# Kernel optimization log

Measured on AMD Instinct MI355X. Metric: run time of the kernel, lower is better.

Reference implementation:

```python
import jax, jax.numpy as jnp
import numpy as np

B, C, T, V, P = 32, 64, 512, 54, 4
EPS = 1e-5


def setup_inputs() -> dict:
    key = jax.random.key(0)
    ks = jax.random.split(key, 5)
    x = jax.random.normal(ks[0], (B, C, T, V), dtype=jnp.float32)
    A = jax.random.uniform(ks[1], (P, V, V), dtype=jnp.float32)
    gweights = jax.random.normal(ks[2], (P, V, V), dtype=jnp.float32)
    W = jax.random.normal(ks[3], (P, C, C), dtype=jnp.float32) * 0.05  # (P, C_out, C_in)
    b = jax.random.normal(ks[4], (P, C), dtype=jnp.float32) * 0.05
    gamma = jnp.ones((C,), dtype=jnp.float32)
    beta = jnp.zeros((C,), dtype=jnp.float32)
    return {"x": x, "A": A, "gweights": gweights, "W": W, "b": b,
            "gamma": gamma, "beta": beta}


def reference(x, A, gweights, W, b, gamma, beta):
    # x: (B, C_in, T, V)
    Aeff = A * gweights  # (P, V, V), learned-weighted adjacency
    # per-part graph aggregation (x @ A_p) followed by 1x1 conv, summed over parts
    # out[b,o,t,v] = sum_p sum_c sum_u x[b,c,t,u] * Aeff[p,u,v] * W[p,o,c] + sum_p b[p,o]
    y = jnp.einsum('bctu,puv,poc->botv', x, Aeff, W, optimize=True)
    y = y + jnp.sum(b, axis=0)[None, :, None, None]
    # BatchNorm2d in training mode: batch stats over (B, T, V) per channel
    mean = jnp.mean(y, axis=(0, 2, 3), keepdims=True)
    var = jnp.mean(jnp.square(y - mean), axis=(0, 2, 3), keepdims=True)
    y = (y - mean) * jax.lax.rsqrt(var + EPS)
    y = y * gamma[None, :, None, None] + beta[None, :, None, None]
    y = jax.nn.relu(y)
    # temporal_conv is Identity (kernel_size=None); residual shortcut is Identity (C_in==C_out)
    return y + x
```

## Files before the change

### kernel.cpp

```cpp
#include <hip/hip_runtime.h>
#include <hip/hip_bf16.h>


typedef __bf16 bf16_t;
typedef __bf16 bf16x8 __attribute__((ext_vector_type(8)));
typedef float  f32x4  __attribute__((ext_vector_type(4)));

#define XT_STRIDE 72
#define UP_STRIDE 232

static __device__ __forceinline__ f32x4 mfma16(bf16x8 a, bf16x8 b, f32x4 c) {
  return __builtin_amdgcn_mfma_f32_16x16x32_bf16(a, b, c, 0, 0, 0);
}

__global__ __launch_bounds__(256) void k_prep(
    const float* __restrict__ A, const float* __restrict__ g,
    const float* __restrict__ W, const float* __restrict__ bias,
    bf16_t* __restrict__ Wstk, bf16_t* __restrict__ At,
    float* __restrict__ bsum, float* __restrict__ stats) {
  int i = blockIdx.x * 256 + threadIdx.x;
  if (i < 16384) Wstk[i] = (bf16_t)W[i];
  if (i < 64 * 224) {
    int v = i / 224, pu = i - v * 224;
    float val = 0.f;
    if (v < 54 && pu < 216) { int idx = pu * 54 + v; val = A[idx] * g[idx]; }
    At[i] = (bf16_t)val;
  }
  if (i < 64) {
    float s = 0.f;
    for (int p = 0; p < 4; ++p) s += bias[p * 64 + i];
    bsum[i] = s;
  }
  if (i < 8192) stats[i] = 0.f;
}

__global__ __launch_bounds__(256) void k_pass1(
    const float* __restrict__ x, const bf16_t* __restrict__ Wstk,
    const bf16_t* __restrict__ At, const float* __restrict__ bsum,
    float* __restrict__ ypre, float* __restrict__ stats) {
  __shared__ bf16_t XtS[4 * 54 * XT_STRIDE];
  __shared__ bf16_t UpS[64 * UP_STRIDE];

  const int tid  = threadIdx.x;
  const int bid  = blockIdx.x;
  const int b    = bid >> 7;
  const int t0   = (bid & 127) << 2;
  const int w    = tid >> 6;
  const int L    = tid & 63;
  const int quad = L >> 4;
  const int l15  = L & 15;

  for (int i = tid; i < 64 * 8; i += 256)
    UpS[(i >> 3) * UP_STRIDE + 216 + (i & 7)] = (bf16_t)0.0f;

  const float* xb = x + (size_t)(b * 64 * 512 + t0) * 54;
  for (int j = tid; j < 64 * 216; j += 256) {
    int c = j / 216;
    int r = j - c * 216;
    float v = xb[(size_t)c * 27648 + r];
    int tt = r / 54;
    int u  = r - tt * 54;
    XtS[(tt * 54 + u) * XT_STRIDE + c] = (bf16_t)v;
  }

  bf16x8 wfr[4][2];
  #pragma unroll
  for (int mi = 0; mi < 4; ++mi) {
    const bf16_t* arow = Wstk + (((((w << 2) + mi) << 4) + l15) * 64) + (quad << 3);
    #pragma unroll
    for (int kk = 0; kk < 2; ++kk)
      wfr[mi][kk] = *(const bf16x8*)(arow + kk * 32);
  }

  const int obase = (w << 4) + (quad << 2);
  float bs[4];
  #pragma unroll
  for (int r = 0; r < 4; ++r) bs[r] = bsum[obase + r];

  bf16x8 zf;
  #pragma unroll
  for (int j = 0; j < 8; ++j) zf[j] = (bf16_t)0.0f;

  float ssum[4] = {0.f, 0.f, 0.f, 0.f};
  float ssq[4]  = {0.f, 0.f, 0.f, 0.f};

  __syncthreads();

  for (int tt = 0; tt < 4; ++tt) {
    bf16x8 xfr[4][2];
    #pragma unroll
    for (int nt = 0; nt < 4; ++nt) {
      const int urow = (nt << 4) + l15;
      #pragma unroll
      for (int kk = 0; kk < 2; ++kk) {
        xfr[nt][kk] = zf;
        if (urow < 54)
          xfr[nt][kk] = *(const bf16x8*)(&XtS[(tt * 54 + urow) * XT_STRIDE + kk * 32 + (quad << 3)]);
      }
    }
    #pragma unroll
    for (int mi = 0; mi < 4; ++mi) {
      f32x4 acc[4];
      #pragma unroll
      for (int nt = 0; nt < 4; ++nt)
        #pragma unroll
        for (int e = 0; e < 4; ++e) acc[nt][e] = 0.f;
      #pragma unroll
      for (int kk = 0; kk < 2; ++kk)
        #pragma unroll
        for (int nt = 0; nt < 4; ++nt)
          acc[nt] = mfma16(wfr[mi][kk], xfr[nt][kk], acc[nt]);
      #pragma unroll
      for (int nt = 0; nt < 4; ++nt) {
        const int u = (nt << 4) + l15;
        if (u < 54) {
          #pragma unroll
          for (int r = 0; r < 4; ++r) {
            int o = (mi << 4) + (quad << 2) + r;
            UpS[o * UP_STRIDE + w * 54 + u] = (bf16_t)acc[nt][r];
          }
        }
      }
    }
    __syncthreads();

    bf16x8 afr[7];
    #pragma unroll
    for (int kk = 0; kk < 7; ++kk)
      afr[kk] = *(const bf16x8*)(&UpS[((w << 4) + l15) * UP_STRIDE + kk * 32 + (quad << 3)]);
    f32x4 acc[4];
    #pragma unroll
    for (int nt = 0; nt < 4; ++nt)
      #pragma unroll
      for (int e = 0; e < 4; ++e) acc[nt][e] = 0.f;
    #pragma unroll
    for (int kk = 0; kk < 7; ++kk) {
      #pragma unroll
      for (int nt = 0; nt < 4; ++nt) {
        bf16x8 bfr = *(const bf16x8*)(At + ((nt << 4) + l15) * 224 + kk * 32 + (quad << 3));
        acc[nt] = mfma16(afr[kk], bfr, acc[nt]);
      }
    }
    const int t = t0 + tt;
    #pragma unroll
    for (int nt = 0; nt < 4; ++nt) {
      const int vcol = (nt << 4) + l15;
      if (vcol < 54) {
        #pragma unroll
        for (int r = 0; r < 4; ++r) {
          float yv = acc[nt][r] + bs[r];
          ypre[(((size_t)b * 64 + (obase + r)) * 512 + t) * 54 + vcol] = yv;
          ssum[r] += yv;
          ssq[r]  += yv * yv;
        }
      }
    }
    __syncthreads();
  }

  #pragma unroll
  for (int off = 1; off < 16; off <<= 1) {
    #pragma unroll
    for (int r = 0; r < 4; ++r) {
      ssum[r] += __shfl_xor(ssum[r], off);
      ssq[r]  += __shfl_xor(ssq[r], off);
    }
  }
  if (l15 == 0) {
    float* sb = stats + (bid & 63) * 128;
    #pragma unroll
    for (int r = 0; r < 4; ++r) {
      atomicAdd(&sb[obase + r], ssum[r]);
      atomicAdd(&sb[64 + obase + r], ssq[r]);
    }
  }
}

__global__ void k_finalize(const float* __restrict__ gamma, const float* __restrict__ beta,
                           const float* __restrict__ stats, float* __restrict__ ac) {
  int o = threadIdx.x;
  if (o >= 64) return;
  float S = 0.f, Q = 0.f;
  for (int buf = 0; buf < 64; ++buf) {
    S += stats[buf * 128 + o];
    Q += stats[buf * 128 + 64 + o];
  }
  const float inv = 1.0f / 884736.0f;
  float mean = S * inv;
  float var  = Q * inv - mean * mean;
  float a = gamma[o] * rsqrtf(var + 1e-5f);
  ac[o]      = a;
  ac[64 + o] = beta[o] - mean * a;
}

__global__ __launch_bounds__(256) void k_pass2(const float* __restrict__ x,
                                               const float* __restrict__ ac,
                                               float* __restrict__ out) {
  size_t i4 = (size_t)blockIdx.x * 256 + threadIdx.x;
  int o = (int)((i4 / 6912) & 63);
  float a = ac[o], c = ac[64 + o];
  float4 yp = ((const float4*)out)[i4];
  float4 xv = ((const float4*)x)[i4];
  float4 res;
  res.x = fmaxf(a * yp.x + c, 0.f) + xv.x;
  res.y = fmaxf(a * yp.y + c, 0.f) + xv.y;
  res.z = fmaxf(a * yp.z + c, 0.f) + xv.z;
  res.w = fmaxf(a * yp.w + c, 0.f) + xv.w;
  ((float4*)out)[i4] = res;
}

extern "C" void kernel_launch(void* const* d_in, const int* in_sizes, int n_in,
                              void* d_out, int out_size, void* d_ws, size_t ws_size,
                              hipStream_t stream) {
  const float* x     = (const float*)d_in[0];
  const float* A     = (const float*)d_in[1];
  const float* g     = (const float*)d_in[2];
  const float* W     = (const float*)d_in[3];
  const float* bias  = (const float*)d_in[4];
  const float* gamma = (const float*)d_in[5];
  const float* beta  = (const float*)d_in[6];

  char* ws = (char*)d_ws;
  bf16_t* Wstk = (bf16_t*)(ws + 0);
  bf16_t* At   = (bf16_t*)(ws + 32768);
  float*  bsum = (float*)(ws + 61440);
  float*  stats= (float*)(ws + 61696);
  float*  ac   = (float*)(ws + 94464);
  float*  out  = (float*)d_out;

  k_prep<<<64, 256, 0, stream>>>(A, g, W, bias, Wstk, At, bsum, stats);
  k_pass1<<<4096, 256, 0, stream>>>(x, Wstk, At, bsum, out, stats);
  k_finalize<<<1, 64, 0, stream>>>(gamma, beta, stats, ac);
  k_pass2<<<55296, 256, 0, stream>>>(x, ac, out);
}
```

Before: 619.6 us.

## Pre-transpose x to bf16 channel-last, store pre-BN output in bf16, restructure pass1

A new transpose kernel converts x into a bf16 (B, T*V, C) layout so pass1 can load MFMA fragments directly from global memory, with no strided fp32 gather or LDS transpose. Pass1 swaps MFMA operand roles, double-buffers the intermediate LDS tile, and writes the pre-normalisation activations as bf16 into workspace, which halves that intermediate traffic in pass1 and pass2. Which path runs depends on workspace size, with fp32 and legacy fallbacks kept. The cost is an extra pass over x plus bf16 rounding of the stored pre-BN values, which lowers accuracy.

```diff
diff --git a/kernel.cpp b/kernel.cpp
--- a/kernel.cpp
+++ b/kernel.cpp
@@ -4,13 +4,17 @@
 
 typedef __bf16 bf16_t;
 typedef __bf16 bf16x8 __attribute__((ext_vector_type(8)));
+typedef __bf16 bf16x4 __attribute__((ext_vector_type(4)));
 typedef float  f32x4  __attribute__((ext_vector_type(4)));
-
-#define XT_STRIDE 72
-#define UP_STRIDE 232
+typedef unsigned int uint32;
 
 static __device__ __forceinline__ f32x4 mfma16(bf16x8 a, bf16x8 b, f32x4 c) {
   return __builtin_amdgcn_mfma_f32_16x16x32_bf16(a, b, c, 0, 0, 0);
+}
+static __device__ __forceinline__ uint32 pk2(float a, float b) {
+  union { __bf16 h; unsigned short u; } ua, ub;
+  ua.h = (__bf16)a; ub.h = (__bf16)b;
+  return (uint32)ua.u | ((uint32)ub.u << 16);
 }
 
 __global__ __launch_bounds__(256) void k_prep(
@@ -34,12 +38,49 @@
   if (i < 8192) stats[i] = 0.f;
 }
 
+__global__ __launch_bounds__(256) void k_tr(const float* __restrict__ x,
+                                            bf16_t* __restrict__ xT) {
+  __shared__ bf16_t T[256 * 66];
+  const int tid = threadIdx.x;
+  const int b = blockIdx.x / 108;
+  const int rblk = blockIdx.x - b * 108;
+  const int r0 = rblk << 8;
+  const float* xb = x + (size_t)b * 64 * 27648 + r0;
+  #pragma unroll 4
+  for (int j = 0; j < 16; ++j) {
+    int idx = tid + (j << 8);
+    int c = idx >> 6, r4 = idx & 63;
+    const float* src = xb + (size_t)c * 27648 + r4;
+    #pragma unroll
+    for (int k = 0; k < 4; ++k) {
+      float v = src[k << 6];
+      T[(r4 + (k << 6)) * 66 + c] = (bf16_t)v;
+    }
+  }
+  __syncthreads();
+  bf16_t* outb = xT + (((size_t)b * 27648 + r0) << 6);
+  const uint32* Td = (const uint32*)T;
+  #pragma unroll
+  for (int j = 0; j < 8; ++j) {
+    int row = (tid >> 3) + (j << 5);
+    int seg = tid & 7;
+    uint32 d0 = Td[row * 33 + (seg << 2) + 0];
+    uint32 d1 = Td[row * 33 + (seg << 2) + 1];
+    uint32 d2 = Td[row * 33 + (seg << 2) + 2];
+    uint32 d3 = Td[row * 33 + (seg << 2) + 3];
+    uint4 vv = make_uint4(d0, d1, d2, d3);
+    *(uint4*)(outb + ((size_t)row << 6) + (seg << 3)) = vv;
+  }
+}
+
+#define UPS 232
+
+template<bool YBF16>
 __global__ __launch_bounds__(256) void k_pass1(
-    const float* __restrict__ x, const bf16_t* __restrict__ Wstk,
+    const bf16_t* __restrict__ xT, const bf16_t* __restrict__ Wstk,
     const bf16_t* __restrict__ At, const float* __restrict__ bsum,
-    float* __restrict__ ypre, float* __restrict__ stats) {
-  __shared__ bf16_t XtS[4 * 54 * XT_STRIDE];
-  __shared__ bf16_t UpS[64 * UP_STRIDE];
+    void* __restrict__ yprev, float* __restrict__ stats) {
+  __shared__ bf16_t UpS[2][64 * UPS];
 
   const int tid  = threadIdx.x;
   const int bid  = blockIdx.x;
@@ -50,42 +91,138 @@
   const int quad = L >> 4;
   const int l15  = L & 15;
 
+  for (int i = tid; i < 1024; i += 256) {
+    int buf = i >> 9, row = (i >> 3) & 63, d = i & 7;
+    ((uint32*)UpS[buf])[row * 116 + 108 + d] = 0u;
+  }
+
+  bf16x8 wb[4][2];
+  #pragma unroll
+  for (int ot = 0; ot < 4; ++ot)
+    #pragma unroll
+    for (int kk = 0; kk < 2; ++kk)
+      wb[ot][kk] = *(const bf16x8*)(Wstk + (((w << 6) + (ot << 4) + l15) << 6)
+                                          + (kk << 5) + (quad << 3));
+
+  const int oc = (w << 4) + l15;
+  const float bsv = bsum[oc];
+  float ssum = 0.f, ssq = 0.f;
+
+  for (int tt = 0; tt < 4; ++tt) {
+    bf16_t* Up = UpS[tt & 1];
+    const int t = t0 + tt;
+
+    const bf16_t* xbase = xT + (((size_t)b * 27648 + (size_t)t * 54) << 6);
+    bf16x8 xa[4][2];
+    #pragma unroll
+    for (int ut = 0; ut < 4; ++ut)
+      #pragma unroll
+      for (int kk = 0; kk < 2; ++kk)
+        xa[ut][kk] = *(const bf16x8*)(xbase + (((ut << 4) + l15) << 6)
+                                            + (kk << 5) + (quad << 3));
+    #pragma unroll
+    for (int ut = 0; ut < 4; ++ut) {
+      const int u0 = (ut << 4) + (quad << 2);
+      #pragma unroll
+      for (int ot = 0; ot < 4; ++ot) {
+        f32x4 acc = {0.f, 0.f, 0.f, 0.f};
+        acc = mfma16(xa[ut][0], wb[ot][0], acc);
+        acc = mfma16(xa[ut][1], wb[ot][1], acc);
+        if (u0 < 54) {
+          uint32* dst = (uint32*)(Up + ((ot << 4) + l15) * UPS + w * 54 + u0);
+          dst[0] = pk2(acc[0], acc[1]);
+          if (u0 + 3 < 54) dst[1] = pk2(acc[2], acc[3]);
+        }
+      }
+    }
+    __syncthreads();
+
+    bf16x8 ub[7];
+    #pragma unroll
+    for (int kk = 0; kk < 7; ++kk)
+      ub[kk] = *(const bf16x8*)(Up + ((w << 4) + l15) * UPS + (kk << 5) + (quad << 3));
+
+    const size_t obase = (((size_t)((b << 6) + oc) << 9) + (size_t)t) * 54;
+    #pragma unroll
+    for (int mi = 0; mi < 4; ++mi) {
+      f32x4 acc = {0.f, 0.f, 0.f, 0.f};
+      #pragma unroll
+      for (int kk = 0; kk < 7; ++kk) {
+        bf16x8 av = *(const bf16x8*)(At + ((mi << 4) + l15) * 224
+                                        + (kk << 5) + (quad << 3));
+        acc = mfma16(av, ub[kk], acc);
+      }
+      const int v0 = (mi << 4) + (quad << 2);
+      if (v0 + 3 < 54) {
+        float y0 = acc[0] + bsv, y1 = acc[1] + bsv, y2 = acc[2] + bsv, y3 = acc[3] + bsv;
+        if (YBF16) {
+          uint32* d = (uint32*)((bf16_t*)yprev + obase + v0);
+          d[0] = pk2(y0, y1); d[1] = pk2(y2, y3);
+        } else {
+          float2* d = (float2*)((float*)yprev + obase + v0);
+          d[0] = make_float2(y0, y1); d[1] = make_float2(y2, y3);
+        }
+        ssum += y0 + y1 + y2 + y3;
+        ssq  += y0 * y0 + y1 * y1 + y2 * y2 + y3 * y3;
+      } else if (v0 == 52) {
+        float y0 = acc[0] + bsv, y1 = acc[1] + bsv;
+        if (YBF16) {
+          *(uint32*)((bf16_t*)yprev + obase + v0) = pk2(y0, y1);
+        } else {
+          *(float2*)((float*)yprev + obase + v0) = make_float2(y0, y1);
+        }
+        ssum += y0 + y1;
+        ssq  += y0 * y0 + y1 * y1;
+      }
+    }
+    __syncthreads();
+  }
+
+  ssum += __shfl_xor(ssum, 16); ssq += __shfl_xor(ssq, 16);
+  ssum += __shfl_xor(ssum, 32); ssq += __shfl_xor(ssq, 32);
+  if (L < 16) {
+    float* sb = stats + (bid & 63) * 128;
+    atomicAdd(&sb[oc], ssum);
+    atomicAdd(&sb[64 + oc], ssq);
+  }
+}
+
+#define XT_STRIDE 72
+#define UP_STRIDE 232
+__global__ __launch_bounds__(256) void k_pass1_legacy(
+    const float* __restrict__ x, const bf16_t* __restrict__ Wstk,
+    const bf16_t* __restrict__ At, const float* __restrict__ bsum,
+    float* __restrict__ ypre, float* __restrict__ stats) {
+  __shared__ bf16_t XtS[4 * 54 * XT_STRIDE];
+  __shared__ bf16_t UpS[64 * UP_STRIDE];
+  const int tid = threadIdx.x, bid = blockIdx.x;
+  const int b = bid >> 7, t0 = (bid & 127) << 2;
+  const int w = tid >> 6, L = tid & 63, quad = L >> 4, l15 = L & 15;
   for (int i = tid; i < 64 * 8; i += 256)
     UpS[(i >> 3) * UP_STRIDE + 216 + (i & 7)] = (bf16_t)0.0f;
-
   const float* xb = x + (size_t)(b * 64 * 512 + t0) * 54;
   for (int j = tid; j < 64 * 216; j += 256) {
-    int c = j / 216;
-    int r = j - c * 216;
+    int c = j / 216, r = j - c * 216;
     float v = xb[(size_t)c * 27648 + r];
-    int tt = r / 54;
-    int u  = r - tt * 54;
+    int tt = r / 54, u = r - tt * 54;
     XtS[(tt * 54 + u) * XT_STRIDE + c] = (bf16_t)v;
   }
-
   bf16x8 wfr[4][2];
   #pragma unroll
   for (int mi = 0; mi < 4; ++mi) {
     const bf16_t* arow = Wstk + (((((w << 2) + mi) << 4) + l15) * 64) + (quad << 3);
     #pragma unroll
-    for (int kk = 0; kk < 2; ++kk)
-      wfr[mi][kk] = *(const bf16x8*)(arow + kk * 32);
-  }
-
+    for (int kk = 0; kk < 2; ++kk) wfr[mi][kk] = *(const bf16x8*)(arow + kk * 32);
+  }
   const int obase = (w << 4) + (quad << 2);
   float bs[4];
   #pragma unroll
   for (int r = 0; r < 4; ++r) bs[r] = bsum[obase + r];
-
   bf16x8 zf;
   #pragma unroll
   for (int j = 0; j < 8; ++j) zf[j] = (bf16_t)0.0f;
-
-  float ssum[4] = {0.f, 0.f, 0.f, 0.f};
-  float ssq[4]  = {0.f, 0.f, 0.f, 0.f};
-
+  float ssum[4] = {0.f,0.f,0.f,0.f}, ssq[4] = {0.f,0.f,0.f,0.f};
   __syncthreads();
-
   for (int tt = 0; tt < 4; ++tt) {
     bf16x8 xfr[4][2];
     #pragma unroll
@@ -113,17 +250,15 @@
       #pragma unroll
       for (int nt = 0; nt < 4; ++nt) {
         const int u = (nt << 4) + l15;
-        if (u < 54) {
+        if (u < 54)
           #pragma unroll
           for (int r = 0; r < 4; ++r) {
             int o = (mi << 4) + (quad << 2) + r;
             UpS[o * UP_STRIDE + w * 54 + u] = (bf16_t)acc[nt][r];
           }
-        }
       }
     }
     __syncthreads();
-
     bf16x8 afr[7];
     #pragma unroll
     for (int kk = 0; kk < 7; ++kk)
@@ -134,38 +269,33 @@
       #pragma unroll
       for (int e = 0; e < 4; ++e) acc[nt][e] = 0.f;
     #pragma unroll
-    for (int kk = 0; kk < 7; ++kk) {
+    for (int kk = 0; kk < 7; ++kk)
       #pragma unroll
       for (int nt = 0; nt < 4; ++nt) {
         bf16x8 bfr = *(const bf16x8*)(At + ((nt << 4) + l15) * 224 + kk * 32 + (quad << 3));
         acc[nt] = mfma16(afr[kk], bfr, acc[nt]);
       }
-    }
     const int t = t0 + tt;
     #pragma unroll
     for (int nt = 0; nt < 4; ++nt) {
       const int vcol = (nt << 4) + l15;
-      if (vcol < 54) {
+      if (vcol < 54)
         #pragma unroll
         for (int r = 0; r < 4; ++r) {
           float yv = acc[nt][r] + bs[r];
           ypre[(((size_t)b * 64 + (obase + r)) * 512 + t) * 54 + vcol] = yv;
-          ssum[r] += yv;
-          ssq[r]  += yv * yv;
+          ssum[r] += yv; ssq[r] += yv * yv;
         }
-      }
     }
     __syncthreads();
   }
-
-  #pragma unroll
-  for (int off = 1; off < 16; off <<= 1) {
+  #pragma unroll
+  for (int off = 1; off < 16; off <<= 1)
     #pragma unroll
     for (int r = 0; r < 4; ++r) {
       ssum[r] += __shfl_xor(ssum[r], off);
       ssq[r]  += __shfl_xor(ssq[r], off);
     }
-  }
   if (l15 == 0) {
     float* sb = stats + (bid & 63) * 128;
     #pragma unroll
@@ -189,24 +319,34 @@
   float mean = S * inv;
   float var  = Q * inv - mean * mean;
   float a = gamma[o] * rsqrtf(var + 1e-5f);
-  ac[o]      = a;
+  ac[o] = a;
   ac[64 + o] = beta[o] - mean * a;
 }
 
+template<bool YBF16>
 __global__ __launch_bounds__(256) void k_pass2(const float* __restrict__ x,
                                                const float* __restrict__ ac,
+                                               const void* __restrict__ yprev,
                                                float* __restrict__ out) {
-  size_t i4 = (size_t)blockIdx.x * 256 + threadIdx.x;
-  int o = (int)((i4 / 6912) & 63);
-  float a = ac[o], c = ac[64 + o];
-  float4 yp = ((const float4*)out)[i4];
-  float4 xv = ((const float4*)x)[i4];
-  float4 res;
-  res.x = fmaxf(a * yp.x + c, 0.f) + xv.x;
-  res.y = fmaxf(a * yp.y + c, 0.f) + xv.y;
-  res.z = fmaxf(a * yp.z + c, 0.f) + xv.z;
-  res.w = fmaxf(a * yp.w + c, 0.f) + xv.w;
-  ((float4*)out)[i4] = res;
+  const int slab = blockIdx.y;
+  const int o = slab & 63;
+  const size_t base = (size_t)slab * 27648 + (size_t)(((blockIdx.x << 8) + threadIdx.x) << 2);
+  const float a = ac[o], c = ac[64 + o];
+  float y0, y1, y2, y3;
+  if (YBF16) {
+    bf16x4 yp = *(const bf16x4*)((const bf16_t*)yprev + base);
+    y0 = (float)yp[0]; y1 = (float)yp[1]; y2 = (float)yp[2]; y3 = (float)yp[3];
+  } else {
+    float4 yp = *(const float4*)((const float*)yprev + base);
+    y0 = yp.x; y1 = yp.y; y2 = yp.z; y3 = yp.w;
+  }
+  float4 xv = *(const float4*)(x + base);
+  float4 r;
+  r.x = fmaxf(fmaf(a, y0, c), 0.f) + xv.x;
+  r.y = fmaxf(fmaf(a, y1, c), 0.f) + xv.y;
+  r.z = fmaxf(fmaf(a, y2, c), 0.f) + xv.z;
+  r.w = fmaxf(fmaf(a, y3, c), 0.f) + xv.w;
+  *(float4*)(out + base) = r;
 }
 
 extern "C" void kernel_launch(void* const* d_in, const int* in_sizes, int n_in,
@@ -221,15 +361,36 @@
   const float* beta  = (const float*)d_in[6];
 
   char* ws = (char*)d_ws;
-  bf16_t* Wstk = (bf16_t*)(ws + 0);
-  bf16_t* At   = (bf16_t*)(ws + 32768);
-  float*  bsum = (float*)(ws + 61440);
-  float*  stats= (float*)(ws + 61696);
-  float*  ac   = (float*)(ws + 94464);
-  float*  out  = (float*)d_out;
+  bf16_t* Wstk  = (bf16_t*)(ws + 0);
+  bf16_t* At    = (bf16_t*)(ws + 32768);
+  float*  bsum  = (float*)(ws + 61440);
+  float*  stats = (float*)(ws + 61696);
+  float*  ac    = (float*)(ws + 94464);
+  const size_t XT_OFF   = 98304;
+  const size_t XT_BYTES = (size_t)32 * 27648 * 64 * 2;
+  const size_t YP_OFF   = XT_OFF + XT_BYTES;
+  bf16_t* xT = (bf16_t*)(ws + XT_OFF);
+  float*  out = (float*)d_out;
+
+  const size_t need_primary = YP_OFF + XT_BYTES + 4096;
+  const size_t need_fbA     = YP_OFF + 4096;
 
   k_prep<<<64, 256, 0, stream>>>(A, g, W, bias, Wstk, At, bsum, stats);
-  k_pass1<<<4096, 256, 0, stream>>>(x, Wstk, At, bsum, out, stats);
-  k_finalize<<<1, 64, 0, stream>>>(gamma, beta, stats, ac);
-  k_pass2<<<55296, 256, 0, stream>>>(x, ac, out);
-}
+
+  if (ws_size >= need_primary) {
+    bf16_t* ypre = (bf16_t*)(ws + YP_OFF);
+    k_tr<<<3456, 256, 0, stream>>>(x, xT);
+    k_pass1<true><<<4096, 256, 0, stream>>>(xT, Wstk, At, bsum, ypre, stats);
+    k_finalize<<<1, 64, 0, stream>>>(gamma, beta, stats, ac);
+    k_pass2<true><<<dim3(27, 2048), 256, 0, stream>>>(x, ac, ypre, out);
+  } else if (ws_size >= need_fbA) {
+    k_tr<<<3456, 256, 0, stream>>>(x, xT);
+    k_pass1<false><<<4096, 256, 0, stream>>>(xT, Wstk, At, bsum, out, stats);
+    k_finalize<<<1, 64, 0, stream>>>(gamma, beta, stats, ac);
+    k_pass2<false><<<dim3(27, 2048), 256, 0, stream>>>(x, ac, out, out);
+  } else {
+    k_pass1_legacy<<<4096, 256, 0, stream>>>(x, Wstk, At, bsum, out, stats);
+    k_finalize<<<1, 64, 0, stream>>>(gamma, beta, stats, ac);
+    k_pass2<false><<<dim3(27, 2048), 256, 0, stream>>>(x, ac, out, out);
+  }
+}
```

Measured after the change: 610.3 us. No clear change (-1.5%).
